# Kernel optimization log

Measured on AMD Instinct MI355X. Metric: run time of the kernel, lower is better.

The kernel has to match this reference:

```python
import jax, jax.numpy as jnp
import numpy as np

B, C, N, Fd = 8, 64, 256, 128
EPS = 1e-5


def setup_inputs() -> dict:
    key = jax.random.key(0)
    k_h, k_op, k_s, k_q = jax.random.split(key, 4)
    # xavier_uniform bound for [C, 2F, 1] slices: gain*sqrt(6/(fan_in+fan_out)) with fan_in=2F, fan_out=1
    bound = float(np.sqrt(6.0 / (2 * Fd + 1)))
    h = jax.random.normal(k_h, (B, C, N, Fd), dtype=jnp.float32)
    op = jax.random.uniform(k_op, (C, 2 * Fd, 1), minval=-bound, maxval=bound, dtype=jnp.float32)
    op_S = jax.random.uniform(k_s, (C, 2 * Fd, 1), minval=-bound, maxval=bound, dtype=jnp.float32)
    op_Q = jax.random.uniform(k_q, (C, 2 * Fd, 1), minval=-bound, maxval=bound, dtype=jnp.float32)
    gamma = jnp.ones((C,), dtype=jnp.float32)
    beta = jnp.zeros((C,), dtype=jnp.float32)
    return {"h": h, "op": op, "op_S": op_S, "op_Q": op_Q, "gamma": gamma, "beta": beta}


def reference(h, op, op_S, op_Q, gamma, beta):
    # h: [B, C, N, F]
    source = h[:, :, 0:1, :]                              # [B,C,1,F]
    h_src = jnp.broadcast_to(source, h.shape)             # repeat_interleave over N
    h_op = jnp.concatenate([h_src, h], axis=-1)           # [B,C,N,2F]
    # [B,C,N,2F] x [C,2F,1] -> [B,C,N,1]
    attn_op = jax.nn.sigmoid(jnp.einsum('bcnf,cfo->bcno', h_op, op))
    op_mask = (attn_op >= 0.5).astype(h.dtype)            # hard threshold (no grad)
    supp = h * op_mask                                    # [B,C,N,F]
    query = h * (1.0 - op_mask)
    supp_mean = jnp.mean(supp, axis=2, keepdims=True)     # [B,C,1,F]
    query_mean = jnp.mean(query, axis=2, keepdims=True)
    supp_attn = jnp.einsum('bcnf,cfo->bcno', jnp.concatenate([supp_mean, source], axis=-1), op_S)
    query_attn = jnp.einsum('bcnf,cfo->bcno', jnp.concatenate([query_mean, source], axis=-1), op_Q)
    op_attn = jax.nn.softmax(jnp.concatenate([supp_attn, query_attn], axis=-1), axis=-1)  # [B,C,1,2]
    h_opn = supp * op_attn[..., 0:1] + query * op_attn[..., 1:2]  # [B,C,N,F]
    # BatchNorm2d (training-mode batch stats) over (B,N,F) per channel
    mean = jnp.mean(h_opn, axis=(0, 2, 3), keepdims=True)
    var = jnp.var(h_opn, axis=(0, 2, 3), keepdims=True)
    h_bn = (h_opn - mean) * jax.lax.rsqrt(var + EPS)
    h_bn = h_bn * gamma[None, :, None, None] + beta[None, :, None, None]
    return jax.nn.elu(h_bn)
```

## Files before the change

### kernel.cpp

```cpp
#include <hip/hip_runtime.h>
#include <math.h>

#define Bb 8
#define Cc 64
#define Nn 256
#define FD 128
#define SEGS 4
#define ROWS 64
#define TILE (Nn * FD)

typedef float floatx4 __attribute__((ext_vector_type(4)));

__global__ __launch_bounds__(256) void s1(
    const float* __restrict__ h, const float* __restrict__ op,
    const float* __restrict__ opS, const float* __restrict__ opQ,
    unsigned long long* __restrict__ maskbuf, float* __restrict__ bpart) {
  const int blk = blockIdx.x;
  const int bc = blk >> 2, seg = blk & 3;
  const int c = bc & (Cc - 1);
  const float* __restrict__ tile = h + (size_t)bc * TILE;
  const int tid = threadIdx.x, lane = tid & 63, wv = tid >> 6;
  const int hw = tid >> 5, hl = tid & 31;

  __shared__ float s_dh[ROWS];
  __shared__ float s_red[4][6];
  __shared__ float s_cs;
  __shared__ float s_ssq[2];

  if (wv == 0) {
    const float* __restrict__ opc = op + c * 2 * FD;
    const float a = tile[lane], b = tile[lane + 64];
    float cs = a * opc[lane] + b * opc[lane + 64];
    float ssv = 0.0f, qqv = 0.0f;
    if (seg == 0) {
      const float* __restrict__ opSc = opS + c * 2 * FD + FD;
      const float* __restrict__ opQc = opQ + c * 2 * FD + FD;
      ssv = a * opSc[lane] + b * opSc[lane + 64];
      qqv = a * opQc[lane] + b * opQc[lane + 64];
    }
#pragma unroll
    for (int off = 32; off >= 1; off >>= 1) {
      cs  += __shfl_xor(cs,  off, 64);
      ssv += __shfl_xor(ssv, off, 64);
      qqv += __shfl_xor(qqv, off, 64);
    }
    if (lane == 0) { s_cs = cs; s_ssq[0] = ssv; s_ssq[1] = qqv; }
  }

  const float4 oH = ((const float4*)(op  + c * 2 * FD + FD))[hl];
  const float4 oS = ((const float4*)(opS + c * 2 * FD))[hl];
  const float4 oQ = ((const float4*)(opQ + c * 2 * FD))[hl];

  float dsp[8], dqp[8], rsp[8], rssp[8];

#pragma unroll
  for (int i = 0; i < 8; ++i) {
    const int nl = hw * 8 + i;
    const float4 v = ((const float4*)(tile + (size_t)(seg * ROWS + nl) * FD))[hl];
    float dh = v.x * oH.x + v.y * oH.y + v.z * oH.z + v.w * oH.w;
    dsp[i]  = v.x * oS.x + v.y * oS.y + v.z * oS.z + v.w * oS.w;
    dqp[i]  = v.x * oQ.x + v.y * oQ.y + v.z * oQ.z + v.w * oQ.w;
    rsp[i]  = v.x + v.y + v.z + v.w;
    rssp[i] = v.x * v.x + v.y * v.y + v.z * v.z + v.w * v.w;
#pragma unroll
    for (int off = 16; off >= 1; off >>= 1) dh += __shfl_xor(dh, off, 64);
    if (hl == 0) s_dh[nl] = dh;
  }
  __syncthreads();

  const float cs = s_cs;

  if (wv == 0) {
    const bool m = (s_dh[lane] + cs) >= 0.0f;
    const unsigned long long bits = __ballot(m);
    if (lane == 0) maskbuf[blk] = bits;
  }

  float a_ds = 0, a_dq = 0, a_rsm = 0, a_rsq = 0, a_rssm = 0, a_rssq = 0;
#pragma unroll
  for (int i = 0; i < 8; ++i) {
    const bool m = (s_dh[hw * 8 + i] + cs) >= 0.0f;
    a_ds   += m ? dsp[i]  : 0.0f;
    a_dq   += m ? 0.0f    : dqp[i];
    a_rsm  += m ? rsp[i]  : 0.0f;
    a_rsq  += m ? 0.0f    : rsp[i];
    a_rssm += m ? rssp[i] : 0.0f;
    a_rssq += m ? 0.0f    : rssp[i];
  }
#pragma unroll
  for (int off = 32; off >= 1; off >>= 1) {
    a_ds   += __shfl_xor(a_ds,   off, 64);
    a_dq   += __shfl_xor(a_dq,   off, 64);
    a_rsm  += __shfl_xor(a_rsm,  off, 64);
    a_rsq  += __shfl_xor(a_rsq,  off, 64);
    a_rssm += __shfl_xor(a_rssm, off, 64);
    a_rssq += __shfl_xor(a_rssq, off, 64);
  }
  if (lane == 0) {
    s_red[wv][0] = a_ds;  s_red[wv][1] = a_dq;
    s_red[wv][2] = a_rsm; s_red[wv][3] = a_rsq;
    s_red[wv][4] = a_rssm; s_red[wv][5] = a_rssq;
  }
  __syncthreads();
  if (tid < 6) {
    bpart[(size_t)blk * 8 + tid] =
        s_red[0][tid] + s_red[1][tid] + s_red[2][tid] + s_red[3][tid];
  }
  if (seg == 0 && tid >= 6 && tid < 8) {
    bpart[(size_t)blk * 8 + tid] = s_ssq[tid - 6];
  }
}

__global__ __launch_bounds__(256) void s2f(
    const float* __restrict__ h, const unsigned long long* __restrict__ maskbuf,
    const float* __restrict__ bpart, const float* __restrict__ gamma,
    const float* __restrict__ beta, float* __restrict__ out) {
  const int blk = blockIdx.x, bc = blk >> 2, seg = blk & 3;
  const int c = bc & (Cc - 1), bmine = bc >> 6;
  const int tid = threadIdx.x, lane = tid & 63, hw = tid >> 5, hl = tid & 31;
  __shared__ float s_S[Bb], s_SS[Bb], s_ws[2 * Bb];
  __shared__ float s_a[ROWS];

  const int b = hw;
  const int bcb = b * Cc + c;

  float aj = 0.0f;
  if (hl < 6) {
#pragma unroll
    for (int k = 0; k < SEGS; ++k)
      aj += bpart[(size_t)(bcb * SEGS + k) * 8 + hl];
  } else if (hl < 8) {
    aj = bpart[(size_t)(bcb * SEGS) * 8 + hl];
  }
  const int base = lane & 32;
  float a0 = __shfl(aj, base + 0, 64), a1 = __shfl(aj, base + 1, 64);
  float a2 = __shfl(aj, base + 2, 64), a3 = __shfl(aj, base + 3, 64);
  float a4 = __shfl(aj, base + 4, 64), a5 = __shfl(aj, base + 5, 64);
  float ss = __shfl(aj, base + 6, 64), qq = __shfl(aj, base + 7, 64);

  float sa = a0 * (1.0f / Nn) + ss;
  float qa = a1 * (1.0f / Nn) + qq;
  float mx = fmaxf(sa, qa);
  float es = __expf(sa - mx), eq = __expf(qa - mx);
  float inv = 1.0f / (es + eq);
  float w_s = es * inv, w_q = eq * inv;
  if (hl == 0) {
    s_S[b]  = w_s * a2 + w_q * a3;
    s_SS[b] = w_s * w_s * a4 + w_q * w_q * a5;
    s_ws[2 * b] = w_s; s_ws[2 * b + 1] = w_q;
  }
  __syncthreads();

  float S = 0.0f, SS = 0.0f;
#pragma unroll
  for (int k = 0; k < Bb; ++k) { S += s_S[k]; SS += s_SS[k]; }
  const float invcnt = 1.0f / (float)(Bb * Nn * FD);
  const float mean = S * invcnt;
  const float var  = SS * invcnt - mean * mean;
  const float scale = gamma[c] * rsqrtf(var + 1e-5f);
  const float shift = beta[c] - mean * scale;

  if (tid < ROWS) {
    const unsigned long long m = maskbuf[blk];
    const float w = ((m >> tid) & 1ull) ? s_ws[2 * bmine] : s_ws[2 * bmine + 1];
    s_a[tid] = w * scale;
  }
  __syncthreads();

  const float4* __restrict__ h4 = (const float4*)(h + (size_t)bc * TILE) + seg * 2048;
  floatx4* __restrict__ o4 = (floatx4*)(out + (size_t)bc * TILE) + seg * 2048;
#pragma unroll
  for (int k = 0; k < 8; ++k) {
    const int idx = k * 256 + tid;
    const float a = s_a[idx >> 5];
    float4 v = h4[idx];
    floatx4 r;
    r.x = fmaf(v.x, a, shift);
    r.y = fmaf(v.y, a, shift);
    r.z = fmaf(v.z, a, shift);
    r.w = fmaf(v.w, a, shift);
    r.x = r.x > 0.0f ? r.x : __expf(r.x) - 1.0f;
    r.y = r.y > 0.0f ? r.y : __expf(r.y) - 1.0f;
    r.z = r.z > 0.0f ? r.z : __expf(r.z) - 1.0f;
    r.w = r.w > 0.0f ? r.w : __expf(r.w) - 1.0f;
    __builtin_nontemporal_store(r, &o4[idx]);
  }
}

extern "C" void kernel_launch(void* const* d_in, const int* in_sizes, int n_in,
                              void* d_out, int out_size, void* d_ws, size_t ws_size,
                              hipStream_t stream) {
  const float* h     = (const float*)d_in[0];
  const float* op    = (const float*)d_in[1];
  const float* opS   = (const float*)d_in[2];
  const float* opQ   = (const float*)d_in[3];
  const float* gamma = (const float*)d_in[4];
  const float* beta  = (const float*)d_in[5];
  float* out = (float*)d_out;

  unsigned long long* maskbuf = (unsigned long long*)d_ws;
  float* bpart = (float*)((char*)d_ws + 16384);

  s1<<<Bb * Cc * SEGS, 256, 0, stream>>>(h, op, opS, opQ, maskbuf, bpart);
  s2f<<<Bb * Cc * SEGS, 256, 0, stream>>>(h, maskbuf, bpart, gamma, beta, out);
}
```

Before: 132.6 us.

## Fuse two stages into one kernel with per-channel atomic barrier

```diff
diff --git a/kernel.cpp b/kernel.cpp
--- a/kernel.cpp
+++ b/kernel.cpp
@@ -8,16 +8,20 @@
 #define SEGS 4
 #define ROWS 64
 #define TILE (Nn * FD)
+#define NBLK (Bb * Cc * SEGS)
+#define SPIN_MAX 2000000
 
 typedef float floatx4 __attribute__((ext_vector_type(4)));
 
-__global__ __launch_bounds__(256) void s1(
+__global__ __launch_bounds__(256) void pipe(
     const float* __restrict__ h, const float* __restrict__ op,
     const float* __restrict__ opS, const float* __restrict__ opQ,
-    unsigned long long* __restrict__ maskbuf, float* __restrict__ bpart) {
+    const float* __restrict__ gamma, const float* __restrict__ beta,
+    float* __restrict__ out, float* __restrict__ bpart,
+    unsigned int* __restrict__ done) {
   const int blk = blockIdx.x;
-  const int bc = blk >> 2, seg = blk & 3;
-  const int c = bc & (Cc - 1);
+  const int c = blk >> 5, b = (blk >> 2) & (Bb - 1), seg = blk & 3;
+  const int bc = b * Cc + c;
   const float* __restrict__ tile = h + (size_t)bc * TILE;
   const int tid = threadIdx.x, lane = tid & 63, wv = tid >> 6;
   const int hw = tid >> 5, hl = tid & 31;
@@ -26,17 +30,20 @@
   __shared__ float s_red[4][6];
   __shared__ float s_cs;
   __shared__ float s_ssq[2];
+  __shared__ unsigned long long s_mask;
+  __shared__ float s_S[Bb], s_SS[Bb], s_ws[2];
+  __shared__ float s_a[ROWS];
 
   if (wv == 0) {
     const float* __restrict__ opc = op + c * 2 * FD;
-    const float a = tile[lane], b = tile[lane + 64];
-    float cs = a * opc[lane] + b * opc[lane + 64];
+    const float a = tile[lane], bb2 = tile[lane + 64];
+    float cs = a * opc[lane] + bb2 * opc[lane + 64];
     float ssv = 0.0f, qqv = 0.0f;
     if (seg == 0) {
       const float* __restrict__ opSc = opS + c * 2 * FD + FD;
       const float* __restrict__ opQc = opQ + c * 2 * FD + FD;
-      ssv = a * opSc[lane] + b * opSc[lane + 64];
-      qqv = a * opQc[lane] + b * opQc[lane + 64];
+      ssv = a * opSc[lane] + bb2 * opSc[lane + 64];
+      qqv = a * opQc[lane] + bb2 * opQc[lane + 64];
     }
 #pragma unroll
     for (int off = 32; off >= 1; off >>= 1) {
@@ -73,7 +80,7 @@
   if (wv == 0) {
     const bool m = (s_dh[lane] + cs) >= 0.0f;
     const unsigned long long bits = __ballot(m);
-    if (lane == 0) maskbuf[blk] = bits;
+    if (lane == 0) s_mask = bits;
   }
 
   float a_ds = 0, a_dq = 0, a_rsm = 0, a_rsq = 0, a_rssm = 0, a_rssq = 0;
@@ -109,45 +116,45 @@
   if (seg == 0 && tid >= 6 && tid < 8) {
     bpart[(size_t)blk * 8 + tid] = s_ssq[tid - 6];
   }
-}
-
-__global__ __launch_bounds__(256) void s2f(
-    const float* __restrict__ h, const unsigned long long* __restrict__ maskbuf,
-    const float* __restrict__ bpart, const float* __restrict__ gamma,
-    const float* __restrict__ beta, float* __restrict__ out) {
-  const int blk = blockIdx.x, bc = blk >> 2, seg = blk & 3;
-  const int c = bc & (Cc - 1), bmine = bc >> 6;
-  const int tid = threadIdx.x, lane = tid & 63, hw = tid >> 5, hl = tid & 31;
-  __shared__ float s_S[Bb], s_SS[Bb], s_ws[2 * Bb];
-  __shared__ float s_a[ROWS];
-
-  const int b = hw;
-  const int bcb = b * Cc + c;
-
+
+  __syncthreads();
+  if (tid == 0) {
+    __hip_atomic_fetch_add(&done[c], 1u, __ATOMIC_RELEASE,
+                           __HIP_MEMORY_SCOPE_AGENT);
+    int it = 0;
+    while (__hip_atomic_load(&done[c], __ATOMIC_ACQUIRE,
+                             __HIP_MEMORY_SCOPE_AGENT) < 32u) {
+      if (++it > SPIN_MAX) break;
+      __builtin_amdgcn_s_sleep(2);
+    }
+  }
+  __syncthreads();
+
+  const int bb = hw;
   float aj = 0.0f;
   if (hl < 6) {
 #pragma unroll
     for (int k = 0; k < SEGS; ++k)
-      aj += bpart[(size_t)(bcb * SEGS + k) * 8 + hl];
+      aj += bpart[(size_t)(c * 32 + bb * 4 + k) * 8 + hl];
   } else if (hl < 8) {
-    aj = bpart[(size_t)(bcb * SEGS) * 8 + hl];
+    aj = bpart[(size_t)(c * 32 + bb * 4) * 8 + hl];
   }
   const int base = lane & 32;
-  float a0 = __shfl(aj, base + 0, 64), a1 = __shfl(aj, base + 1, 64);
-  float a2 = __shfl(aj, base + 2, 64), a3 = __shfl(aj, base + 3, 64);
-  float a4 = __shfl(aj, base + 4, 64), a5 = __shfl(aj, base + 5, 64);
-  float ss = __shfl(aj, base + 6, 64), qq = __shfl(aj, base + 7, 64);
-
-  float sa = a0 * (1.0f / Nn) + ss;
-  float qa = a1 * (1.0f / Nn) + qq;
-  float mx = fmaxf(sa, qa);
-  float es = __expf(sa - mx), eq = __expf(qa - mx);
-  float inv = 1.0f / (es + eq);
-  float w_s = es * inv, w_q = eq * inv;
+  const float a0 = __shfl(aj, base + 0, 64), a1 = __shfl(aj, base + 1, 64);
+  const float a2 = __shfl(aj, base + 2, 64), a3 = __shfl(aj, base + 3, 64);
+  const float a4 = __shfl(aj, base + 4, 64), a5 = __shfl(aj, base + 5, 64);
+  const float ss = __shfl(aj, base + 6, 64), qq = __shfl(aj, base + 7, 64);
+
+  const float sa = a0 * (1.0f / Nn) + ss;
+  const float qa = a1 * (1.0f / Nn) + qq;
+  const float mx = fmaxf(sa, qa);
+  const float es = __expf(sa - mx), eq = __expf(qa - mx);
+  const float inv = 1.0f / (es + eq);
+  const float w_s = es * inv, w_q = eq * inv;
   if (hl == 0) {
-    s_S[b]  = w_s * a2 + w_q * a3;
-    s_SS[b] = w_s * w_s * a4 + w_q * w_q * a5;
-    s_ws[2 * b] = w_s; s_ws[2 * b + 1] = w_q;
+    s_S[bb]  = w_s * a2 + w_q * a3;
+    s_SS[bb] = w_s * w_s * a4 + w_q * w_q * a5;
+    if (bb == b) { s_ws[0] = w_s; s_ws[1] = w_q; }
   }
   __syncthreads();
 
@@ -161,19 +168,18 @@
   const float shift = beta[c] - mean * scale;
 
   if (tid < ROWS) {
-    const unsigned long long m = maskbuf[blk];
-    const float w = ((m >> tid) & 1ull) ? s_ws[2 * bmine] : s_ws[2 * bmine + 1];
+    const float w = ((s_mask >> tid) & 1ull) ? s_ws[0] : s_ws[1];
     s_a[tid] = w * scale;
   }
   __syncthreads();
 
-  const float4* __restrict__ h4 = (const float4*)(h + (size_t)bc * TILE) + seg * 2048;
+  const float4* __restrict__ h4 = (const float4*)tile + seg * 2048;
   floatx4* __restrict__ o4 = (floatx4*)(out + (size_t)bc * TILE) + seg * 2048;
 #pragma unroll
   for (int k = 0; k < 8; ++k) {
     const int idx = k * 256 + tid;
     const float a = s_a[idx >> 5];
-    float4 v = h4[idx];
+    const float4 v = h4[idx];
     floatx4 r;
     r.x = fmaf(v.x, a, shift);
     r.y = fmaf(v.y, a, shift);
@@ -198,9 +204,10 @@
   const float* beta  = (const float*)d_in[5];
   float* out = (float*)d_out;
 
-  unsigned long long* maskbuf = (unsigned long long*)d_ws;
-  float* bpart = (float*)((char*)d_ws + 16384);
-
-  s1<<<Bb * Cc * SEGS, 256, 0, stream>>>(h, op, opS, opQ, maskbuf, bpart);
-  s2f<<<Bb * Cc * SEGS, 256, 0, stream>>>(h, maskbuf, bpart, gamma, beta, out);
+  float* bpart = (float*)d_ws;
+  unsigned int* done = (unsigned int*)((char*)d_ws + 65536);
+
+  hipMemsetAsync(done, 0, Cc * sizeof(unsigned int), stream);
+  pipe<<<NBLK, 256, 0, stream>>>(h, op, opS, opQ, gamma, beta, out,
+                                 bpart, done);
 }
```

Result: slower. 273.0 us (+105.8%).
